# Kernel tuning notes

Hardware: AMD Instinct MI355X
Metric: run time of the kernel (lower is better)

Reference implementation:

```python
import jax, jax.numpy as jnp
import numpy as np

D_MODEL = 64
HEADS = 8
LEVELS = 5
POINTS = 4
DH = D_MODEL // HEADS
EPS = 1e-5


def _layernorm(x, g, b):
    m = x.mean(-1, keepdims=True)
    v = ((x - m) ** 2).mean(-1, keepdims=True)
    return (x - m) / jnp.sqrt(v + EPS) * g + b


def _bilinear_sample(v, lx, ly, Hl, Wl):
    # v: (B, heads, Hl, Wl, dh); lx, ly: (B, Nq, heads, P) normalized in ~[0,1]
    # matches F.grid_sample(align_corners=False, padding_mode='zeros')
    x = lx * Wl - 0.5
    y = ly * Hl - 0.5
    x0 = jnp.floor(x)
    y0 = jnp.floor(y)
    wx = x - x0
    wy = y - y0
    x0i = x0.astype(jnp.int32)
    y0i = y0.astype(jnp.int32)
    B, heads = v.shape[0], v.shape[1]
    bidx = jnp.arange(B)[:, None, None, None]
    hidx = jnp.arange(heads)[None, None, :, None]

    def gather(yi, xi):
        valid = (xi >= 0) & (xi < Wl) & (yi >= 0) & (yi < Hl)
        xc = jnp.clip(xi, 0, Wl - 1)
        yc = jnp.clip(yi, 0, Hl - 1)
        g = v[bidx, hidx, yc, xc]  # (B, Nq, heads, P, dh)
        return g * valid[..., None].astype(v.dtype)

    return (gather(y0i, x0i) * ((1 - wx) * (1 - wy))[..., None]
            + gather(y0i, x0i + 1) * (wx * (1 - wy))[..., None]
            + gather(y0i + 1, x0i) * ((1 - wx) * wy)[..., None]
            + gather(y0i + 1, x0i + 1) * (wx * wy)[..., None])


def setup_inputs() -> dict:
    key = jax.random.key(0)
    ks = jax.random.split(key, 24)
    B, NQ = 2, 20000
    ss = np.array([[184, 184], [92, 92], [46, 46], [23, 23], [12, 12]], dtype=np.int64)
    areas = ss[:, 0] * ss[:, 1]
    lsi = np.concatenate([[0], np.cumsum(areas)[:-1]]).astype(np.int64)
    LIN = int(areas.sum())  # 45109
    s = 0.02
    inp = {
        'q_feat': jax.random.normal(ks[0], (B, NQ, D_MODEL), jnp.float32),
        'dense_voxel_flatten': jax.random.normal(ks[1], (B, LIN, D_MODEL), jnp.float32),
        'reference_points': jax.random.uniform(ks[2], (B, NQ, 2), jnp.float32),
        'q_pos': jax.random.normal(ks[3], (B, NQ, D_MODEL), jnp.float32),
        'spatial_shapes': ss,
        'level_start_index': lsi,
        'Wv': jax.random.normal(ks[4], (D_MODEL, D_MODEL), jnp.float32) * s,
        'bv': jnp.zeros((D_MODEL,), jnp.float32),
        'Wo': jax.random.normal(ks[5], (D_MODEL, HEADS * LEVELS * POINTS * 2), jnp.float32) * s,
        'bo': jax.random.normal(ks[6], (HEADS * LEVELS * POINTS * 2,), jnp.float32),
        'Wa': jax.random.normal(ks[7], (D_MODEL, HEADS * LEVELS * POINTS), jnp.float32) * s,
        'ba': jnp.zeros((HEADS * LEVELS * POINTS,), jnp.float32),
        'Wout': jax.random.normal(ks[8], (D_MODEL, D_MODEL), jnp.float32) * s,
        'bout': jnp.zeros((D_MODEL,), jnp.float32),
        'g1': jnp.ones((D_MODEL,), jnp.float32),
        'b1': jnp.zeros((D_MODEL,), jnp.float32),
        'W1': jax.random.normal(ks[9], (D_MODEL, 1024), jnp.float32) * s,
        'bff1': jnp.zeros((1024,), jnp.float32),
        'W2': jax.random.normal(ks[10], (1024, D_MODEL), jnp.float32) * s,
        'bff2': jnp.zeros((D_MODEL,), jnp.float32),
        'g2': jnp.ones((D_MODEL,), jnp.float32),
        'b2': jnp.zeros((D_MODEL,), jnp.float32),
    }
    return inp


def reference(q_feat, dense_voxel_flatten, reference_points, q_pos,
              spatial_shapes, level_start_index,
              Wv, bv, Wo, bo, Wa, ba, Wout, bout,
              g1, b1, W1, bff1, W2, bff2, g2, b2):
    B, NQ, _ = q_feat.shape
    q = q_feat + q_pos  # with_pos_embed
    value = (dense_voxel_flatten @ Wv + bv).reshape(B, -1, HEADS, DH)
    off = (q @ Wo + bo).reshape(B, NQ, HEADS, LEVELS, POINTS, 2)
    aw = jax.nn.softmax((q @ Wa + ba).reshape(B, NQ, HEADS, LEVELS * POINTS), axis=-1)
    aw = aw.reshape(B, NQ, HEADS, LEVELS, POINTS)
    # offset normalizer is (W, H) per level
    ssn = np.asarray(spatial_shapes)
    normalizer = jnp.asarray(ssn[:, ::-1].copy(), q.dtype)  # (L, 2)
    loc = reference_points[:, :, None, None, None, :] + off / normalizer[None, None, None, :, None, :]
    out = jnp.zeros((B, NQ, HEADS, DH), q.dtype)
    for l in range(LEVELS):
        Hl, Wl = int(ssn[l, 0]), int(ssn[l, 1])
        st = int(np.asarray(level_start_index)[l])
        vl = value[:, st:st + Hl * Wl].reshape(B, Hl, Wl, HEADS, DH).transpose(0, 3, 1, 2, 4)
        sampled = _bilinear_sample(vl, loc[:, :, :, l, :, 0], loc[:, :, :, l, :, 1], Hl, Wl)
        out = out + jnp.einsum('bnhpd,bnhp->bnhd', sampled, aw[:, :, :, l])
    attn_out = out.reshape(B, NQ, D_MODEL) @ Wout + bout
    x = _layernorm(q_feat + attn_out, g1, b1)  # residual + norm1 (dropout=0)
    ffn = jax.nn.relu(x @ W1 + bff1) @ W2 + bff2
    return _layernorm(x + ffn, g2, b2)
```

## Files before the change

### kernel.cpp

```cpp
#include <hip/hip_runtime.h>
#include <hip/hip_bf16.h>

#define NB 2
#define NQ 20000
#define DM 64
#define NH 8
#define NL 5
#define NP 4
#define LIN 45109
#define FFN 1024

typedef __attribute__((ext_vector_type(8))) short short8;
typedef __attribute__((ext_vector_type(4))) float f32x4;

__device__ __forceinline__ float b2f(const __hip_bfloat16 h) { return __bfloat162float(h); }
__device__ __forceinline__ float lo16f(unsigned u) { return __uint_as_float(u << 16); }
__device__ __forceinline__ float hi16f(unsigned u) { return __uint_as_float(u & 0xffff0000u); }
__device__ __forceinline__ unsigned f2bf_bits(float x) {
    unsigned u = __float_as_uint(x);
    return (u + 0x7FFFu + ((u >> 16) & 1u)) >> 16;
}

__global__ void __launch_bounds__(256)
val_proj_kernel(const float* __restrict__ dvf,
                const float* __restrict__ Wv,
                const float* __restrict__ bv,
                __hip_bfloat16* __restrict__ valA,
                __hip_bfloat16* __restrict__ valB,
                int rows) {
    __shared__ __align__(16) __hip_bfloat16 wvp[8][64][8];
    __shared__ __align__(16) __hip_bfloat16 ar[64][72];
    __shared__ __align__(16) float bvs[64];

    const int tid = threadIdx.x;
    const int lane = tid & 63;
    const int w = tid >> 6;
    const int m16 = lane & 15, qd = lane >> 4;
    const int row0 = blockIdx.x * 64;

    for (int idx = tid; idx < 4096; idx += 256) {
        const int j = idx & 7;
        const int l = (idx >> 3) & 63;
        const int seg = idx >> 9;
        const int nt = seg >> 1, kc = seg & 1;
        const int n = nt * 16 + (l & 15);
        const int k = kc * 32 + (l >> 4) * 8 + j;
        wvp[seg][l][j] = __float2bfloat16(Wv[k * 64 + n]);
    }
    if (tid < 64) bvs[tid] = bv[tid];

    {
        const int r = w * 16 + m16;
        const int grow = row0 + r;
        const int c0 = qd * 16;
        __hip_bfloat16* dst = &ar[r][c0];
        if (grow < rows) {
            const float4* src = (const float4*)&dvf[(size_t)grow * DM + c0];
#pragma unroll
            for (int t = 0; t < 4; t++) {
                const float4 v = src[t];
                dst[t * 4 + 0] = __float2bfloat16(v.x);
                dst[t * 4 + 1] = __float2bfloat16(v.y);
                dst[t * 4 + 2] = __float2bfloat16(v.z);
                dst[t * 4 + 3] = __float2bfloat16(v.w);
            }
        } else {
#pragma unroll
            for (int t = 0; t < 16; t++) dst[t] = __float2bfloat16(0.f);
        }
    }
    __syncthreads();

    f32x4 acc[4];
#pragma unroll
    for (int mt = 0; mt < 4; mt++) acc[mt] = (f32x4){0.f, 0.f, 0.f, 0.f};
#pragma unroll
    for (int kc = 0; kc < 2; kc++) {
        const short8 b = *(const short8*)&ar[w * 16 + m16][kc * 32 + qd * 8];
#pragma unroll
        for (int mt = 0; mt < 4; mt++) {
            const short8 a = *(const short8*)&wvp[mt * 2 + kc][lane][0];
            acc[mt] = __builtin_amdgcn_mfma_f32_16x16x32_bf16(a, b, acc[mt], 0, 0, 0);
        }
    }

    {
        const int vg = row0 + w * 16 + m16;
        if (vg < rows) {
            const int vr = (vg < LIN) ? vg : vg - LIN;
            __hip_bfloat16* dst = (vg < LIN) ? valA : valB;
#pragma unroll
            for (int mt = 0; mt < 4; mt++) {
                const int c0 = mt * 16 + qd * 4;
                const float4 bv4 = *(const float4*)&bvs[c0];
                const float r0 = acc[mt][0] + bv4.x, r1 = acc[mt][1] + bv4.y;
                const float r2 = acc[mt][2] + bv4.z, r3 = acc[mt][3] + bv4.w;
                uint2 u;
                u.x = f2bf_bits(r0) | (f2bf_bits(r1) << 16);
                u.y = f2bf_bits(r2) | (f2bf_bits(r3) << 16);
                *(uint2*)&dst[((size_t)(c0 >> 3) * LIN + vr) * 8 + (c0 & 7)] = u;
            }
        }
    }
}

__global__ void pack_kernel(const float* __restrict__ W1, const float* __restrict__ W2,
                            const float* __restrict__ Wo, const float* __restrict__ Wa,
                            const float* __restrict__ Wout,
                            __hip_bfloat16* __restrict__ W1p, __hip_bfloat16* __restrict__ W2p,
                            __hip_bfloat16* __restrict__ Woap, __hip_bfloat16* __restrict__ Woutp) {
    const int t = blockIdx.x * 256 + threadIdx.x;
    const int lane = t & 63;
    const int m = lane & 15, qd = lane >> 4;
    const int seg = t >> 6;
    if (seg < 128) {
        const int nt = seg >> 1, kc = seg & 1;
        const int n = nt * 16 + m, kb = kc * 32 + qd * 8;
        __hip_bfloat16* dst = W1p + ((size_t)seg * 64 + lane) * 8;
#pragma unroll
        for (int j = 0; j < 8; j++) dst[j] = __float2bfloat16(W1[(size_t)(kb + j) * FFN + n]);
    } else if (seg < 256) {
        const int sl = seg - 128;
        const int nt = sl >> 5, kc = sl & 31;
        const int n = nt * 16 + m, kb = kc * 32 + qd * 8;
        __hip_bfloat16* dst = W2p + ((size_t)sl * 64 + lane) * 8;
#pragma unroll
        for (int j = 0; j < 8; j++) dst[j] = __float2bfloat16(W2[(size_t)(kb + j) * DM + n]);
    } else if (seg < 316) {
        const int sl = seg - 256;
        const int nt = sl >> 1, kc = sl & 1;
        const int n = nt * 16 + m, kb = kc * 32 + qd * 8;
        __hip_bfloat16* dst = Woap + ((size_t)sl * 64 + lane) * 8;
#pragma unroll
        for (int j = 0; j < 8; j++) {
            const int k = kb + j;
            const float v = (n < 320) ? Wo[(size_t)k * 320 + n] : Wa[(size_t)k * 160 + (n - 320)];
            dst[j] = __float2bfloat16(v);
        }
    } else if (seg < 324) {
        const int sl = seg - 316;
        const int nt = sl >> 1, kc = sl & 1;
        const int n = nt * 16 + m, kb = kc * 32 + qd * 8;
        __hip_bfloat16* dst = Woutp + ((size_t)sl * 64 + lane) * 8;
#pragma unroll
        for (int j = 0; j < 8; j++) dst[j] = __float2bfloat16(Wout[(size_t)(kb + j) * DM + n]);
    }
}

__global__ void __launch_bounds__(256, 8)
attn4_kernel(const float* __restrict__ q_feat,
             const float* __restrict__ ref_pts,
             const float* __restrict__ q_pos,
             const __hip_bfloat16* __restrict__ Woap,
             const float* __restrict__ bo, const float* __restrict__ ba,
             const __hip_bfloat16* __restrict__ Woutp, const float* __restrict__ bout,
             const float* __restrict__ g1, const float* __restrict__ b1,
             const __hip_bfloat16* __restrict__ valA,
             const __hip_bfloat16* __restrict__ valB,
             int qoff,
             float* __restrict__ xout) {
    __shared__ __align__(16) __hip_bfloat16 qb[16][72];
    __shared__ __align__(16) float offs[4][321];
    __shared__ __align__(16) float aws[4][161];
    __shared__ __align__(16) float refs[4][2];
    __shared__ __align__(16) int4  dsc[640];

    float (*xs4)[64] = (float(*)[64])offs;

    const int tid = threadIdx.x;
    const int lane = tid & 63;
    const int w = tid >> 6;
    const int m16 = lane & 15, qd = lane >> 4;
    const int q0 = qoff + blockIdx.x * 4;
    const int qi = q0 + w;

    const int sz[NL]  = {184, 92, 46, 23, 12};
    const int lsi[NL] = {0, 33856, 42320, 44436, 44965};

    const __hip_bfloat16* valp = (q0 >= NQ) ? valB : valA;

    const float qf = q_feat[(size_t)qi * DM + lane];
    const float qp = q_pos[(size_t)qi * DM + lane];
    qb[w][lane] = __float2bfloat16(qf + qp);
    for (int idx = tid; idx < 12 * 16; idx += 256)
        *(uint2*)&qb[4 + (idx >> 4)][(idx & 15) * 4] = (uint2){0u, 0u};
    if (tid < 8) refs[tid >> 1][tid & 1] = ref_pts[(size_t)(q0 + (tid >> 1)) * 2 + (tid & 1)];
    __syncthreads();

    for (int nt = w; nt < 30; nt += 4) {
        f32x4 acc = {0.f, 0.f, 0.f, 0.f};
#pragma unroll
        for (int kc = 0; kc < 2; kc++) {
            const short8 a = *(const short8*)&qb[m16][kc * 32 + qd * 8];
            const short8 b = *(const short8*)(Woap + ((size_t)(nt * 2 + kc) * 64 + lane) * 8);
            acc = __builtin_amdgcn_mfma_f32_16x16x32_bf16(a, b, acc, 0, 0, 0);
        }
        if (qd == 0) {
            const int n = nt * 16 + m16;
            if (n < 320) {
                const float bn = bo[n];
#pragma unroll
                for (int r = 0; r < 4; r++) offs[r][n] = acc[r] + bn;
            } else {
                const float bn = ba[n - 320];
#pragma unroll
                for (int r = 0; r < 4; r++) aws[r][n - 320] = acc[r] + bn;
            }
        }
    }
    __syncthreads();

    {
        const int g = tid >> 3;
        const int q = g >> 3, h = g & 7;
        const int j = tid & 7;
        float* p = &aws[q][h * 20];
        const float v0 = p[j], v1 = p[j + 8];
        const float v2 = (j < 4) ? p[j + 16] : -1e30f;
        float mx = fmaxf(fmaxf(v0, v1), v2);
        mx = fmaxf(mx, __shfl_xor(mx, 1, 8));
        mx = fmaxf(mx, __shfl_xor(mx, 2, 8));
        mx = fmaxf(mx, __shfl_xor(mx, 4, 8));
        const float e0 = __expf(v0 - mx), e1 = __expf(v1 - mx);
        const float e2 = (j < 4) ? __expf(v2 - mx) : 0.f;
        float s = e0 + e1 + e2;
        s += __shfl_xor(s, 1, 8);
        s += __shfl_xor(s, 2, 8);
        s += __shfl_xor(s, 4, 8);
        const float inv = 1.f / s;
        p[j] = e0 * inv;
        p[j + 8] = e1 * inv;
        if (j < 4) p[j + 16] = e2 * inv;
    }
    __syncthreads();

    for (int s = tid; s < 640; s += 256) {
        const int h = s & 7;
        const int t2 = s >> 3;
        const int p = t2 & 3;
        const int t3 = t2 >> 2;
        const int l = t3 % 5;
        const int q = t3 / 5;
        const int Wl = sz[l];
        const float Wf = (float)Wl;
        const int st = lsi[l];
        const int c = ((h * 5 + l) * 4 + p) * 2;
        const float fx = fmaf(refs[q][0], Wf, offs[q][c]) - 0.5f;
        const float fy = fmaf(refs[q][1], Wf, offs[q][c + 1]) - 0.5f;
        const float x0f = floorf(fx), y0f = floorf(fy);
        const float wx = fx - x0f, wy = fy - y0f;
        const int x0 = (int)x0f, y0 = (int)y0f;
        const float aV = aws[q][h * 20 + l * 4 + p];
        const bool xin0 = (x0 >= 0) & (x0 < Wl);
        const bool xin1 = (x0 >= -1) & (x0 < Wl - 1);
        const bool yin0 = (y0 >= 0) & (y0 < Wl);
        const bool yin1 = (y0 >= -1) & (y0 < Wl - 1);
        const float w00 = (xin0 & yin0) ? (1.f - wx) * (1.f - wy) * aV : 0.f;
        const float w10 = (xin1 & yin0) ? wx * (1.f - wy) * aV : 0.f;
        const float w01 = (xin0 & yin1) ? (1.f - wx) * wy * aV : 0.f;
        const float w11 = (xin1 & yin1) ? wx * wy * aV : 0.f;
        int b0 = (st + y0 * Wl + x0) * 8;
        b0 = b0 < -1520 ? -1520 : b0;
        b0 = b0 > LIN * 8 ? LIN * 8 : b0;
        const int b1i = b0 + Wl * 8;
        int4 d4;
        d4.x = b0;
        d4.y = b1i;
        d4.z = (int)(f2bf_bits(w00) | (f2bf_bits(w10) << 16));
        d4.w = (int)(f2bf_bits(w01) | (f2bf_bits(w11) << 16));
        dsc[s] = d4;
    }
    __syncthreads();

    {
        const int h = lane >> 3, j = lane & 7;
        const int c = j & 3;
        const int sp = j >> 2;
        const __hip_bfloat16* vbase = valp + (size_t)h * (LIN * 8);
        float acc[8] = {0.f, 0.f, 0.f, 0.f, 0.f, 0.f, 0.f, 0.f};
#pragma unroll
        for (int k = 0; k < 10; k++) {
            const int s = 2 * k + sp;
            const int4 d4 = dsc[(w * 20 + s) * 8 + h];
            const int base = (c >= 2) ? d4.y : d4.x;
            const unsigned wb = (unsigned)((c >= 2) ? d4.w : d4.z);
            const float wt = (c & 1) ? hi16f(wb) : lo16f(wb);
            const short8 v = *(const short8*)(vbase + base + (c & 1) * 8);
#pragma unroll
            for (int d = 0; d < 8; d++)
                acc[d] = fmaf(wt, __uint_as_float(((unsigned)(unsigned short)v[d]) << 16), acc[d]);
        }
        const bool hi4 = (j & 4) != 0;
        float k4[4], gv4[4];
#pragma unroll
        for (int d = 0; d < 4; d++) {
            k4[d] = hi4 ? acc[d + 4] : acc[d];
            gv4[d] = hi4 ? acc[d] : acc[d + 4];
        }
#pragma unroll
        for (int d = 0; d < 4; d++) k4[d] += __shfl_xor(gv4[d], 4, 64);
        const bool hi2 = (j & 2) != 0;
        float k2[2], gv2[2];
#pragma unroll
        for (int d = 0; d < 2; d++) {
            k2[d] = hi2 ? k4[d + 2] : k4[d];
            gv2[d] = hi2 ? k4[d] : k4[d + 2];
        }
#pragma unroll
        for (int d = 0; d < 2; d++) k2[d] += __shfl_xor(gv2[d], 2, 64);
        const bool hi1 = (j & 1) != 0;
        float k1 = hi1 ? k2[1] : k2[0];
        float gv1 = hi1 ? k2[0] : k2[1];
        k1 += __shfl_xor(gv1, 1, 64);
        qb[w][lane] = __float2bfloat16(k1);
    }
    __syncthreads();

    {
        f32x4 acc = {0.f, 0.f, 0.f, 0.f};
#pragma unroll
        for (int kc = 0; kc < 2; kc++) {
            const short8 a = *(const short8*)&qb[m16][kc * 32 + qd * 8];
            const short8 b = *(const short8*)(Woutp + ((size_t)(w * 2 + kc) * 64 + lane) * 8);
            acc = __builtin_amdgcn_mfma_f32_16x16x32_bf16(a, b, acc, 0, 0, 0);
        }
        if (qd == 0) {
            const int n = w * 16 + m16;
            const float bn = bout[n];
#pragma unroll
            for (int r = 0; r < 4; r++) xs4[r][n] = acc[r] + bn;
        }
    }
    __syncthreads();

    {
        const float xpre = qf + xs4[w][lane];
        float s = xpre, s2 = xpre * xpre;
#pragma unroll
        for (int o = 32; o >= 1; o >>= 1) {
            s += __shfl_xor(s, o, 64);
            s2 += __shfl_xor(s2, o, 64);
        }
        const float mean = s * (1.f / 64.f);
        const float var = s2 * (1.f / 64.f) - mean * mean;
        const float xn = (xpre - mean) * rsqrtf(var + 1e-5f);
        xout[(size_t)qi * DM + lane] = xn * g1[lane] + b1[lane];
    }
}

__global__ void __launch_bounds__(256)
ffn_kernel(const __hip_bfloat16* __restrict__ W1p, const float* __restrict__ bff1,
           const __hip_bfloat16* __restrict__ W2p, const float* __restrict__ bff2,
           const float* __restrict__ g2, const float* __restrict__ b2,
           float* __restrict__ io) {
    __shared__ __align__(16) __hip_bfloat16 xq[2][2][64][8];
    __shared__ __align__(16) __hip_bfloat16 hb[32][264];
    __shared__ __align__(16) float yr[32][64];

    const int tid = threadIdx.x;
    const int lane = tid & 63;
    const int w = tid >> 6;
    const int m16 = lane & 15, qd = lane >> 4;
    const int q0 = blockIdx.x * 32;

    {
        const int q = tid >> 3, i = tid & 7;
        const float4 v0 = *(const float4*)&io[(size_t)(q0 + q) * DM + i * 8];
        const float4 v1 = *(const float4*)&io[(size_t)(q0 + q) * DM + i * 8 + 4];
        uint2 ua, ub;
        ua.x = f2bf_bits(v0.x) | (f2bf_bits(v0.y) << 16);
        ua.y = f2bf_bits(v0.z) | (f2bf_bits(v0.w) << 16);
        ub.x = f2bf_bits(v1.x) | (f2bf_bits(v1.y) << 16);
        ub.y = f2bf_bits(v1.z) | (f2bf_bits(v1.w) << 16);
        uint4 u4 = {ua.x, ua.y, ub.x, ub.y};
        *(uint4*)&xq[q >> 4][i >> 2][(q & 15) + (i & 3) * 16][0] = u4;
    }
    __syncthreads();

    short8 bx[2][2];
#pragma unroll
    for (int nt = 0; nt < 2; nt++)
#pragma unroll
        for (int kc = 0; kc < 2; kc++)
            bx[nt][kc] = *(const short8*)&xq[nt][kc][lane][0];

    f32x4 yacc[2];
    yacc[0] = (f32x4){0.f, 0.f, 0.f, 0.f};
    yacc[1] = (f32x4){0.f, 0.f, 0.f, 0.f};

#pragma unroll
    for (int qtr = 0; qtr < 4; qtr++) {
#pragma unroll
        for (int mt = 0; mt < 4; mt++) {
            const int htl = mt * 4 + w;
            const int ht = qtr * 16 + htl;
            f32x4 acc[2];
            acc[0] = (f32x4){0.f, 0.f, 0.f, 0.f};
            acc[1] = (f32x4){0.f, 0.f, 0.f, 0.f};
#pragma unroll
            for (int kc = 0; kc < 2; kc++) {
                const short8 a = *(const short8*)(W1p + ((size_t)(ht * 2 + kc) * 64 + lane) * 8);
#pragma unroll
                for (int nt = 0; nt < 2; nt++)
                    acc[nt] = __builtin_amdgcn_mfma_f32_16x16x32_bf16(a, bx[nt][kc], acc[nt], 0, 0, 0);
            }
            const float4 b4 = *(const float4*)&bff1[ht * 16 + qd * 4];
#pragma unroll
            for (int nt = 0; nt < 2; nt++) {
                const float r0 = fmaxf(acc[nt][0] + b4.x, 0.f);
                const float r1 = fmaxf(acc[nt][1] + b4.y, 0.f);
                const float r2 = fmaxf(acc[nt][2] + b4.z, 0.f);
                const float r3 = fmaxf(acc[nt][3] + b4.w, 0.f);
                uint2 u;
                u.x = f2bf_bits(r0) | (f2bf_bits(r1) << 16);
                u.y = f2bf_bits(r2) | (f2bf_bits(r3) << 16);
                *(uint2*)&hb[nt * 16 + m16][htl * 16 + qd * 4] = u;
            }
        }
        __syncthreads();
#pragma unroll
        for (int kc2 = 0; kc2 < 8; kc2++) {
            const short8 b = *(const short8*)(W2p + ((size_t)(w * 32 + qtr * 8 + kc2) * 64 + lane) * 8);
#pragma unroll
            for (int mt = 0; mt < 2; mt++) {
                const short8 a = *(const short8*)&hb[mt * 16 + m16][kc2 * 32 + qd * 8];
                yacc[mt] = __builtin_amdgcn_mfma_f32_16x16x32_bf16(a, b, yacc[mt], 0, 0, 0);
            }
        }
        __syncthreads();
    }

    {
        const int n = w * 16 + m16;
        const float bn = bff2[n];
#pragma unroll
        for (int mt = 0; mt < 2; mt++)
#pragma unroll
            for (int r = 0; r < 4; r++) {
                const int mm = mt * 16 + qd * 4 + r;
                yr[mm][n] = yacc[mt][r] + bn;
            }
    }
    __syncthreads();

    {
        const int q = tid >> 3, i = tid & 7;
        const float4 x0 = *(const float4*)&io[(size_t)(q0 + q) * DM + i * 8];
        const float4 x1 = *(const float4*)&io[(size_t)(q0 + q) * DM + i * 8 + 4];
        float4 v0 = *(const float4*)&yr[q][i * 8];
        float4 v1 = *(const float4*)&yr[q][i * 8 + 4];
        v0.x += x0.x; v0.y += x0.y; v0.z += x0.z; v0.w += x0.w;
        v1.x += x1.x; v1.y += x1.y; v1.z += x1.z; v1.w += x1.w;
        float s = v0.x + v0.y + v0.z + v0.w + v1.x + v1.y + v1.z + v1.w;
        float s2 = v0.x * v0.x + v0.y * v0.y + v0.z * v0.z + v0.w * v0.w
                 + v1.x * v1.x + v1.y * v1.y + v1.z * v1.z + v1.w * v1.w;
#pragma unroll
        for (int o = 4; o >= 1; o >>= 1) { s += __shfl_xor(s, o, 64); s2 += __shfl_xor(s2, o, 64); }
        const float mean = s * (1.f / 64.f);
        const float var = s2 * (1.f / 64.f) - mean * mean;
        const float rstd = rsqrtf(var + 1e-5f);
        const float4 ga = *(const float4*)&g2[i * 8];
        const float4 gb = *(const float4*)&g2[i * 8 + 4];
        const float4 ba4 = *(const float4*)&b2[i * 8];
        const float4 bb4 = *(const float4*)&b2[i * 8 + 4];
        float4 o0, o1;
        o0.x = (v0.x - mean) * rstd * ga.x + ba4.x;
        o0.y = (v0.y - mean) * rstd * ga.y + ba4.y;
        o0.z = (v0.z - mean) * rstd * ga.z + ba4.z;
        o0.w = (v0.w - mean) * rstd * ga.w + ba4.w;
        o1.x = (v1.x - mean) * rstd * gb.x + bb4.x;
        o1.y = (v1.y - mean) * rstd * gb.y + bb4.y;
        o1.z = (v1.z - mean) * rstd * gb.z + bb4.z;
        o1.w = (v1.w - mean) * rstd * gb.w + bb4.w;
        *(float4*)&io[(size_t)(q0 + q) * DM + i * 8] = o0;
        *(float4*)&io[(size_t)(q0 + q) * DM + i * 8 + 4] = o1;
    }
}

extern "C" void kernel_launch(void* const* d_in, const int* in_sizes, int n_in,
                              void* d_out, int out_size, void* d_ws, size_t ws_size,
                              hipStream_t stream) {
    const int B0 = (in_sizes[4] >= 4096) ? 4 : 6;
    const float* q_feat = (const float*)d_in[0];
    const float* dvf    = (const float*)d_in[1];
    const float* refp   = (const float*)d_in[2];
    const float* q_pos  = (const float*)d_in[3];
    const float* Wv   = (const float*)d_in[B0 + 0];
    const float* bv   = (const float*)d_in[B0 + 1];
    const float* Wo   = (const float*)d_in[B0 + 2];
    const float* bo   = (const float*)d_in[B0 + 3];
    const float* Wa   = (const float*)d_in[B0 + 4];
    const float* ba   = (const float*)d_in[B0 + 5];
    const float* Wout = (const float*)d_in[B0 + 6];
    const float* bout = (const float*)d_in[B0 + 7];
    const float* g1   = (const float*)d_in[B0 + 8];
    const float* b1   = (const float*)d_in[B0 + 9];
    const float* W1   = (const float*)d_in[B0 + 10];
    const float* bff1 = (const float*)d_in[B0 + 11];
    const float* W2   = (const float*)d_in[B0 + 12];
    const float* bff2 = (const float*)d_in[B0 + 13];
    const float* g2   = (const float*)d_in[B0 + 14];
    const float* b2   = (const float*)d_in[B0 + 15];
    float* out = (float*)d_out;

    const size_t val_elems = (size_t)LIN * DM;
    const size_t pack_elems = (size_t)(128 + 128 + 60 + 8) * 64 * 8;
    const size_t PAD_ELEMS = 12288;
    const bool dbuf = ws_size >= (pack_elems + 2 * val_elems + PAD_ELEMS) * sizeof(__hip_bfloat16);

    __hip_bfloat16* W1p = (__hip_bfloat16*)d_ws;
    __hip_bfloat16* W2p = W1p + (size_t)128 * 64 * 8;
    __hip_bfloat16* Woap = W2p + (size_t)128 * 64 * 8;
    __hip_bfloat16* Woutp = Woap + (size_t)60 * 64 * 8;
    __hip_bfloat16* val0 = W1p + pack_elems;
    __hip_bfloat16* val1 = dbuf ? val0 + val_elems : val0;

    __hip_bfloat16* pad_ptr = val1 + val_elems;
    hipMemsetAsync(pad_ptr, 0, PAD_ELEMS * sizeof(__hip_bfloat16), stream);

    pack_kernel<<<81, 256, 0, stream>>>(W1, W2, Wo, Wa, Wout, W1p, W2p, Woap, Woutp);

    if (dbuf) {
        val_proj_kernel<<<(2 * LIN + 63) / 64, 256, 0, stream>>>(
            dvf, Wv, bv, val0, val1, 2 * LIN);
        attn4_kernel<<<(NB * NQ) / 4, 256, 0, stream>>>(
            q_feat, refp, q_pos, Woap, bo, ba, Woutp, bout, g1, b1,
            val0, val1, 0, out);
    } else {
        for (int b = 0; b < NB; b++) {
            val_proj_kernel<<<(LIN + 63) / 64, 256, 0, stream>>>(
                dvf + (size_t)b * val_elems, Wv, bv, val0, val0, LIN);
            attn4_kernel<<<NQ / 4, 256, 0, stream>>>(
                q_feat, refp, q_pos, Woap, bo, ba, Woutp, bout, g1, b1,
                val0, val0, b * NQ, out);
        }
    }
    ffn_kernel<<<(NB * NQ) / 32, 256, 0, stream>>>(W1p, bff1, W2p, bff2, g2, b2, out);
}
```

Baseline: 234.0 us.

## Fuse weight packing, pad memset and value projection into one prep kernel; batch gathers

Merges the weight-packing kernel, the pad-zeroing memset and the value projection into a single launch, using block-index ranges, so two launches and a memset disappear. In the attention kernel the query A-fragments are loaded once and the offset/weight GEMM loop is unrolled. The bilinear gather loop now issues five value loads before consuming them, giving more memory-level parallelism at the cost of more registers. The fallback (non-double-buffer) path now repacks weights on every batch iteration.

```diff
diff --git a/kernel.cpp b/kernel.cpp
--- a/kernel.cpp
+++ b/kernel.cpp
@@ -22,21 +22,71 @@
 }
 
 __global__ void __launch_bounds__(256)
-val_proj_kernel(const float* __restrict__ dvf,
-                const float* __restrict__ Wv,
-                const float* __restrict__ bv,
-                __hip_bfloat16* __restrict__ valA,
-                __hip_bfloat16* __restrict__ valB,
-                int rows) {
+prep_kernel(const float* __restrict__ dvf,
+            const float* __restrict__ Wv, const float* __restrict__ bv,
+            const float* __restrict__ W1, const float* __restrict__ W2,
+            const float* __restrict__ Wo, const float* __restrict__ Wa,
+            const float* __restrict__ Wout,
+            __hip_bfloat16* __restrict__ W1p, __hip_bfloat16* __restrict__ W2p,
+            __hip_bfloat16* __restrict__ Woap, __hip_bfloat16* __restrict__ Woutp,
+            __hip_bfloat16* __restrict__ valA, __hip_bfloat16* __restrict__ valB,
+            __hip_bfloat16* __restrict__ pad_ptr,
+            int rows) {
     __shared__ __align__(16) __hip_bfloat16 wvp[8][64][8];
     __shared__ __align__(16) __hip_bfloat16 ar[64][72];
     __shared__ __align__(16) float bvs[64];
 
     const int tid = threadIdx.x;
+    const int bid = blockIdx.x;
     const int lane = tid & 63;
     const int w = tid >> 6;
     const int m16 = lane & 15, qd = lane >> 4;
-    const int row0 = blockIdx.x * 64;
+
+    if (bid < 81) {
+        const int t = bid * 256 + tid;
+        const int m = m16;
+        const int seg = t >> 6;
+        if (seg < 128) {
+            const int nt = seg >> 1, kc = seg & 1;
+            const int n = nt * 16 + m, kb = kc * 32 + qd * 8;
+            __hip_bfloat16* dst = W1p + ((size_t)seg * 64 + lane) * 8;
+#pragma unroll
+            for (int j = 0; j < 8; j++) dst[j] = __float2bfloat16(W1[(size_t)(kb + j) * FFN + n]);
+        } else if (seg < 256) {
+            const int sl = seg - 128;
+            const int nt = sl >> 5, kc = sl & 31;
+            const int n = nt * 16 + m, kb = kc * 32 + qd * 8;
+            __hip_bfloat16* dst = W2p + ((size_t)sl * 64 + lane) * 8;
+#pragma unroll
+            for (int j = 0; j < 8; j++) dst[j] = __float2bfloat16(W2[(size_t)(kb + j) * DM + n]);
+        } else if (seg < 316) {
+            const int sl = seg - 256;
+            const int nt = sl >> 1, kc = sl & 1;
+            const int n = nt * 16 + m, kb = kc * 32 + qd * 8;
+            __hip_bfloat16* dst = Woap + ((size_t)sl * 64 + lane) * 8;
+#pragma unroll
+            for (int j = 0; j < 8; j++) {
+                const int k = kb + j;
+                const float v = (n < 320) ? Wo[(size_t)k * 320 + n] : Wa[(size_t)k * 160 + (n - 320)];
+                dst[j] = __float2bfloat16(v);
+            }
+        } else if (seg < 324) {
+            const int sl = seg - 316;
+            const int nt = sl >> 1, kc = sl & 1;
+            const int n = nt * 16 + m, kb = kc * 32 + qd * 8;
+            __hip_bfloat16* dst = Woutp + ((size_t)sl * 64 + lane) * 8;
+#pragma unroll
+            for (int j = 0; j < 8; j++) dst[j] = __float2bfloat16(Wout[(size_t)(kb + j) * DM + n]);
+        }
+        return;
+    }
+    if (bid == 81) {
+        uint4* p = (uint4*)pad_ptr;
+        for (int i = tid; i < 1536; i += 256) p[i] = (uint4){0u, 0u, 0u, 0u};
+        return;
+    }
+
+    const int row0 = (bid - 82) * 64;
 
     for (int idx = tid; idx < 4096; idx += 256) {
         const int j = idx & 7;
@@ -101,49 +151,6 @@
                 *(uint2*)&dst[((size_t)(c0 >> 3) * LIN + vr) * 8 + (c0 & 7)] = u;
             }
         }
-    }
-}
-
-__global__ void pack_kernel(const float* __restrict__ W1, const float* __restrict__ W2,
-                            const float* __restrict__ Wo, const float* __restrict__ Wa,
-                            const float* __restrict__ Wout,
-                            __hip_bfloat16* __restrict__ W1p, __hip_bfloat16* __restrict__ W2p,
-                            __hip_bfloat16* __restrict__ Woap, __hip_bfloat16* __restrict__ Woutp) {
-    const int t = blockIdx.x * 256 + threadIdx.x;
-    const int lane = t & 63;
-    const int m = lane & 15, qd = lane >> 4;
-    const int seg = t >> 6;
-    if (seg < 128) {
-        const int nt = seg >> 1, kc = seg & 1;
-        const int n = nt * 16 + m, kb = kc * 32 + qd * 8;
-        __hip_bfloat16* dst = W1p + ((size_t)seg * 64 + lane) * 8;
-#pragma unroll
-        for (int j = 0; j < 8; j++) dst[j] = __float2bfloat16(W1[(size_t)(kb + j) * FFN + n]);
-    } else if (seg < 256) {
-        const int sl = seg - 128;
-        const int nt = sl >> 5, kc = sl & 31;
-        const int n = nt * 16 + m, kb = kc * 32 + qd * 8;
-        __hip_bfloat16* dst = W2p + ((size_t)sl * 64 + lane) * 8;
-#pragma unroll
-        for (int j = 0; j < 8; j++) dst[j] = __float2bfloat16(W2[(size_t)(kb + j) * DM + n]);
-    } else if (seg < 316) {
-        const int sl = seg - 256;
-        const int nt = sl >> 1, kc = sl & 1;
-        const int n = nt * 16 + m, kb = kc * 32 + qd * 8;
-        __hip_bfloat16* dst = Woap + ((size_t)sl * 64 + lane) * 8;
-#pragma unroll
-        for (int j = 0; j < 8; j++) {
-            const int k = kb + j;
-            const float v = (n < 320) ? Wo[(size_t)k * 320 + n] : Wa[(size_t)k * 160 + (n - 320)];
-            dst[j] = __float2bfloat16(v);
-        }
-    } else if (seg < 324) {
-        const int sl = seg - 316;
-        const int nt = sl >> 1, kc = sl & 1;
-        const int n = nt * 16 + m, kb = kc * 32 + qd * 8;
-        __hip_bfloat16* dst = Woutp + ((size_t)sl * 64 + lane) * 8;
-#pragma unroll
-        for (int j = 0; j < 8; j++) dst[j] = __float2bfloat16(Wout[(size_t)(kb + j) * DM + n]);
     }
 }
 
@@ -187,24 +194,30 @@
     if (tid < 8) refs[tid >> 1][tid & 1] = ref_pts[(size_t)(q0 + (tid >> 1)) * 2 + (tid & 1)];
     __syncthreads();
 
-    for (int nt = w; nt < 30; nt += 4) {
-        f32x4 acc = {0.f, 0.f, 0.f, 0.f};
-#pragma unroll
-        for (int kc = 0; kc < 2; kc++) {
-            const short8 a = *(const short8*)&qb[m16][kc * 32 + qd * 8];
-            const short8 b = *(const short8*)(Woap + ((size_t)(nt * 2 + kc) * 64 + lane) * 8);
-            acc = __builtin_amdgcn_mfma_f32_16x16x32_bf16(a, b, acc, 0, 0, 0);
-        }
-        if (qd == 0) {
-            const int n = nt * 16 + m16;
-            if (n < 320) {
-                const float bn = bo[n];
-#pragma unroll
-                for (int r = 0; r < 4; r++) offs[r][n] = acc[r] + bn;
-            } else {
-                const float bn = ba[n - 320];
-#pragma unroll
-                for (int r = 0; r < 4; r++) aws[r][n - 320] = acc[r] + bn;
+    {
+        const short8 qa0 = *(const short8*)&qb[m16][qd * 8];
+        const short8 qa1 = *(const short8*)&qb[m16][32 + qd * 8];
+#pragma unroll
+        for (int t = 0; t < 8; t++) {
+            const int nt = w + t * 4;
+            if (nt < 30) {
+                const short8 b0 = *(const short8*)(Woap + ((size_t)(nt * 2 + 0) * 64 + lane) * 8);
+                const short8 b1 = *(const short8*)(Woap + ((size_t)(nt * 2 + 1) * 64 + lane) * 8);
+                f32x4 acc = {0.f, 0.f, 0.f, 0.f};
+                acc = __builtin_amdgcn_mfma_f32_16x16x32_bf16(qa0, b0, acc, 0, 0, 0);
+                acc = __builtin_amdgcn_mfma_f32_16x16x32_bf16(qa1, b1, acc, 0, 0, 0);
+                if (qd == 0) {
+                    const int n = nt * 16 + m16;
+                    if (n < 320) {
+                        const float bn = bo[n];
+#pragma unroll
+                        for (int r = 0; r < 4; r++) offs[r][n] = acc[r] + bn;
+                    } else {
+                        const float bn = ba[n - 320];
+#pragma unroll
+                        for (int r = 0; r < 4; r++) aws[r][n - 320] = acc[r] + bn;
+                    }
+                }
             }
         }
     }
@@ -276,19 +289,27 @@
         const int h = lane >> 3, j = lane & 7;
         const int c = j & 3;
         const int sp = j >> 2;
-        const __hip_bfloat16* vbase = valp + (size_t)h * (LIN * 8);
+        const __hip_bfloat16* vbase = valp + (size_t)h * (LIN * 8) + (c & 1) * 8;
         float acc[8] = {0.f, 0.f, 0.f, 0.f, 0.f, 0.f, 0.f, 0.f};
 #pragma unroll
-        for (int k = 0; k < 10; k++) {
-            const int s = 2 * k + sp;
-            const int4 d4 = dsc[(w * 20 + s) * 8 + h];
-            const int base = (c >= 2) ? d4.y : d4.x;
-            const unsigned wb = (unsigned)((c >= 2) ? d4.w : d4.z);
-            const float wt = (c & 1) ? hi16f(wb) : lo16f(wb);
-            const short8 v = *(const short8*)(vbase + base + (c & 1) * 8);
-#pragma unroll
-            for (int d = 0; d < 8; d++)
-                acc[d] = fmaf(wt, __uint_as_float(((unsigned)(unsigned short)v[d]) << 16), acc[d]);
+        for (int g = 0; g < 2; g++) {
+            short8 v[5];
+            unsigned wb[5];
+#pragma unroll
+            for (int k = 0; k < 5; k++) {
+                const int s = 2 * (g * 5 + k) + sp;
+                const int4 d4 = dsc[(w * 20 + s) * 8 + h];
+                const int base = (c >= 2) ? d4.y : d4.x;
+                wb[k] = (unsigned)((c >= 2) ? d4.w : d4.z);
+                v[k] = *(const short8*)(vbase + base);
+            }
+#pragma unroll
+            for (int k = 0; k < 5; k++) {
+                const float wt = (c & 1) ? hi16f(wb[k]) : lo16f(wb[k]);
+#pragma unroll
+                for (int d = 0; d < 8; d++)
+                    acc[d] = fmaf(wt, __uint_as_float(((unsigned)(unsigned short)v[k][d]) << 16), acc[d]);
+            }
         }
         const bool hi4 = (j & 4) != 0;
         float k4[4], gv4[4];
@@ -514,22 +535,20 @@
     __hip_bfloat16* Woutp = Woap + (size_t)60 * 64 * 8;
     __hip_bfloat16* val0 = W1p + pack_elems;
     __hip_bfloat16* val1 = dbuf ? val0 + val_elems : val0;
-
     __hip_bfloat16* pad_ptr = val1 + val_elems;
-    hipMemsetAsync(pad_ptr, 0, PAD_ELEMS * sizeof(__hip_bfloat16), stream);
-
-    pack_kernel<<<81, 256, 0, stream>>>(W1, W2, Wo, Wa, Wout, W1p, W2p, Woap, Woutp);
 
     if (dbuf) {
-        val_proj_kernel<<<(2 * LIN + 63) / 64, 256, 0, stream>>>(
-            dvf, Wv, bv, val0, val1, 2 * LIN);
+        prep_kernel<<<82 + (2 * LIN + 63) / 64, 256, 0, stream>>>(
+            dvf, Wv, bv, W1, W2, Wo, Wa, Wout,
+            W1p, W2p, Woap, Woutp, val0, val1, pad_ptr, 2 * LIN);
         attn4_kernel<<<(NB * NQ) / 4, 256, 0, stream>>>(
             q_feat, refp, q_pos, Woap, bo, ba, Woutp, bout, g1, b1,
             val0, val1, 0, out);
     } else {
         for (int b = 0; b < NB; b++) {
-            val_proj_kernel<<<(LIN + 63) / 64, 256, 0, stream>>>(
-                dvf + (size_t)b * val_elems, Wv, bv, val0, val0, LIN);
+            prep_kernel<<<82 + (LIN + 63) / 64, 256, 0, stream>>>(
+                dvf + (size_t)b * val_elems, Wv, bv, W1, W2, Wo, Wa, Wout,
+                W1p, W2p, Woap, Woutp, val0, val0, pad_ptr, LIN);
             attn4_kernel<<<NQ / 4, 256, 0, stream>>>(
                 q_feat, refp, q_pos, Woap, bo, ba, Woutp, bout, g1, b1,
                 val0, val0, b * NQ, out);
```

New measurement: 225.1 us. 1.04x faster.
